# Kernel optimization log

Hardware: AMD Instinct MI355X
Metric: run time of the kernel (lower is better)

Reference implementation:

```python
import jax, jax.numpy as jnp
import numpy as np

HEADS = 4
LOCAL_CTX = 8  # local_attn_ctx (stride)


def _strided_transpose(x, n_ctx, local_ctx):
    # [B, n_ctx, E] -> reshape [B, n_ctx//local, local, E] -> swap -> [B, n_ctx, E]
    B, _, E = x.shape
    bT = n_ctx // local_ctx
    return x.reshape(B, bT, local_ctx, E).transpose(0, 2, 1, 3).reshape(B, n_ctx, E)


def _strided_untranspose(a, n_ctx, local_ctx):
    B, _, E = a.shape
    bT = n_ctx // local_ctx
    return a.reshape(B, local_ctx, bT, E).transpose(0, 2, 1, 3).reshape(B, n_ctx, E)


def setup_inputs() -> dict:
    key = jax.random.key(0)
    ks = jax.random.split(key, 6)
    B, T, E = 2048, 64, 256
    value = jax.random.normal(ks[0], (B, T, E), dtype=jnp.float32)
    k_in = jax.random.normal(ks[1], (B, T, E), dtype=jnp.float32)
    query = jax.random.normal(ks[2], (B, T, E), dtype=jnp.float32)
    mask = jnp.ones((B, T), dtype=jnp.int32)  # unused by the block
    W_ff = jax.random.normal(ks[3], (256, T * E), dtype=jnp.float32) * (1.0 / np.sqrt(T * E))
    b_ff = jax.random.normal(ks[4], (256,), dtype=jnp.float32) * 0.01
    return {"value": value, "key": k_in, "query": query, "mask": mask, "W_ff": W_ff, "b_ff": b_ff}


def reference(value, key, query, mask, W_ff, b_ff):
    B, n_ctx, E = query.shape
    # strided transpose of q, k, v
    q = _strided_transpose(query, n_ctx, LOCAL_CTX)
    k = _strided_transpose(key, n_ctx, LOCAL_CTX)
    v = _strided_transpose(value, n_ctx, LOCAL_CTX)
    scale = 1.0 / np.sqrt(E // HEADS)  # n_state = embd // heads
    w = jax.nn.softmax(jnp.einsum('bqe,bke->bqk', q, k) * scale, axis=-1)
    a = jnp.einsum('bqk,bke->bqe', w, v)
    attention = _strided_untranspose(a, n_ctx, LOCAL_CTX)
    # residual + dropout (eval-mode identity)
    x = attention + query
    # flatten-linear + ReLU
    out = jax.nn.relu(x.reshape(B, n_ctx * E) @ W_ff.T + b_ff)
    return (out, attention)
```

## Files before the change

kernel.cpp:

```cpp
#include <hip/hip_runtime.h>
#include <stdint.h>

typedef __attribute__((ext_vector_type(8))) short s16x8;
typedef __attribute__((ext_vector_type(8))) _Float16 h16x8;
typedef __attribute__((ext_vector_type(4))) float f32x4;

__device__ __forceinline__ unsigned short f2h_bits(float f) {
  union { _Float16 h; unsigned short u; } cv;
  cv.h = (_Float16)f;
  return cv.u;
}
__device__ __forceinline__ unsigned short f2bf(float f) {
  unsigned int u = __float_as_uint(f);
  u += 0x7fffu + ((u >> 16) & 1u);
  return (unsigned short)(u >> 16);
}
__device__ __forceinline__ f32x4 mfma16h(h16x8 a, h16x8 b, f32x4 c) {
  return __builtin_amdgcn_mfma_f32_16x16x32_f16(a, b, c, 0, 0, 0);
}

__device__ __forceinline__ void write_vq(char* VqB, int ep2, int tg, const float2* g) {
  s16x8 lo, hi;
#pragma unroll
  for (int j = 0; j < 8; ++j) {
    lo[j] = (short)f2h_bits(g[j].x);
    hi[j] = (short)f2h_bits(g[j].y);
  }
  *(s16x8*)(VqB + ep2 * 128 + ((16 * tg) ^ (((ep2 >> 1) & 7) << 4))) = lo;
  *(s16x8*)(VqB + (ep2 + 1) * 128 + ((16 * tg) ^ (((ep2 >> 1) & 7) << 4))) = hi;
}

__global__ __launch_bounds__(256) void attn_kernel(
    const float* __restrict__ Vg, const float* __restrict__ Kg,
    const float* __restrict__ Qg, float* __restrict__ attn_out,
    unsigned short* __restrict__ xb ) {
  __shared__ __align__(16) char smem[24576];
  char* PLB = smem + 16384;

  const int b = blockIdx.x;
  const int tid = threadIdx.x;
  const int lane = tid & 63;
  const int w = tid >> 6;
  const int n = lane & 15;
  const int q = lane >> 4;

  const float* Qb = Qg + (size_t)b * 64 * 256;
  const float* Kb = Kg + (size_t)b * 64 * 256;
  const float* Vb = Vg + (size_t)b * 64 * 256;

  const int ep2 = (tid & 31) * 2;
  const int tg = tid >> 5;

  f32x4 accS[4];
#pragma unroll
  for (int c = 0; c < 4; ++c) accS[c] = f32x4{0.f, 0.f, 0.f, 0.f};

#pragma unroll
  for (int ph = 0; ph < 2; ++ph) {
    const int e0 = ph * 128;
#pragma unroll
    for (int kk = 0; kk < 4; ++kk) {
      const int cb = kk * 32 + q * 8;
      const float* qsrc = Qb + (16 * w + n) * 256 + e0 + cb;
      float4 q0 = *(const float4*)qsrc;
      float4 q1 = *(const float4*)(qsrc + 4);
      float4 k0[4], k1[4];
#pragma unroll
      for (int c = 0; c < 4; ++c) {
        const float* ksrc = Kb + (16 * c + n) * 256 + e0 + cb;
        k0[c] = *(const float4*)ksrc;
        k1[c] = *(const float4*)(ksrc + 4);
      }
      h16x8 qh;
      qh[0] = (_Float16)q0.x; qh[1] = (_Float16)q0.y;
      qh[2] = (_Float16)q0.z; qh[3] = (_Float16)q0.w;
      qh[4] = (_Float16)q1.x; qh[5] = (_Float16)q1.y;
      qh[6] = (_Float16)q1.z; qh[7] = (_Float16)q1.w;
#pragma unroll
      for (int c = 0; c < 4; ++c) {
        h16x8 kh;
        kh[0] = (_Float16)k0[c].x; kh[1] = (_Float16)k0[c].y;
        kh[2] = (_Float16)k0[c].z; kh[3] = (_Float16)k0[c].w;
        kh[4] = (_Float16)k1[c].x; kh[5] = (_Float16)k1[c].y;
        kh[6] = (_Float16)k1[c].z; kh[7] = (_Float16)k1[c].w;
        accS[c] = mfma16h(qh, kh, accS[c]);
      }
    }
  }

  float2 g0[8], g1[8];
#pragma unroll
  for (int j = 0; j < 8; ++j) g0[j] = *(const float2*)(Vb + (tg * 8 + j) * 256 + 0 + ep2);
#pragma unroll
  for (int j = 0; j < 8; ++j) g1[j] = *(const float2*)(Vb + (tg * 8 + j) * 256 + 64 + ep2);

  const float scale = 0.125f;
  float p[4][4];
#pragma unroll
  for (int r = 0; r < 4; ++r) {
    float m = -1e30f;
#pragma unroll
    for (int c = 0; c < 4; ++c) m = fmaxf(m, accS[c][r]);
#pragma unroll
    for (int mk = 1; mk < 16; mk <<= 1) m = fmaxf(m, __shfl_xor(m, mk, 64));
    float s = 0.f;
#pragma unroll
    for (int c = 0; c < 4; ++c) {
      float e = __expf((accS[c][r] - m) * scale);
      p[c][r] = e;
      s += e;
    }
#pragma unroll
    for (int mk = 1; mk < 16; mk <<= 1) s += __shfl_xor(s, mk, 64);
    float inv = 1.0f / s;
#pragma unroll
    for (int c = 0; c < 4; ++c) p[c][r] *= inv;
  }

#pragma unroll
  for (int r = 0; r < 4; ++r) {
    int row = 16 * w + 4 * q + r;
    int sw = (row & 7) << 4;
#pragma unroll
    for (int c = 0; c < 4; ++c)
      *(unsigned short*)(PLB + row * 128 + ((2 * (16 * c + n)) ^ sw)) =
          f2h_bits(p[c][r]);
  }

  write_vq(smem, ep2, tg, g0);
  __syncthreads();

  float2 g2[8], g3[8];
  f32x4 accA[4];
#pragma unroll
  for (int qi = 0; qi < 4; ++qi) {
    char* VqB = smem + (qi & 1) * 8192;
    if (qi == 0) {
#pragma unroll
      for (int j = 0; j < 8; ++j)
        g2[j] = *(const float2*)(Vb + (tg * 8 + j) * 256 + 128 + ep2);
    }
    if (qi == 1) {
#pragma unroll
      for (int j = 0; j < 8; ++j)
        g3[j] = *(const float2*)(Vb + (tg * 8 + j) * 256 + 192 + ep2);
    }

#pragma unroll
    for (int c = 0; c < 4; ++c) accA[c] = f32x4{0.f, 0.f, 0.f, 0.f};
    __builtin_amdgcn_s_setprio(1);
#pragma unroll
    for (int ks = 0; ks < 2; ++ks) {
      const int cb = (ks * 32 + q * 8) * 2;
      h16x8 af = *(const h16x8*)(PLB + (16 * w + n) * 128 + (cb ^ ((n & 7) << 4)));
#pragma unroll
      for (int c = 0; c < 4; ++c) {
        int row = 16 * c + n;
        h16x8 bf = *(const h16x8*)(VqB + row * 128 + (cb ^ (((row >> 1) & 7) << 4)));
        accA[c] = mfma16h(af, bf, accA[c]);
      }
    }
    __builtin_amdgcn_s_setprio(0);

    if (qi < 3) {
      char* VqN = smem + ((qi + 1) & 1) * 8192;
      if (qi == 0) write_vq(VqN, ep2, tg, g1);
      if (qi == 1) write_vq(VqN, ep2, tg, g2);
      if (qi == 2) write_vq(VqN, ep2, tg, g3);
      __syncthreads();
    }

#pragma unroll
    for (int r = 0; r < 4; ++r) {
      int t = 16 * w + 4 * q + r;
      const float* qrow = Qb + t * 256 + qi * 64;
      size_t base = ((size_t)b * 64 + t) * 256 + qi * 64;
#pragma unroll
      for (int c = 0; c < 4; ++c) {
        int e = 16 * c + n;
        float aval = accA[c][r];
        attn_out[base + e] = aval;
        if (xb) xb[base + e] = f2h_bits(aval + qrow[e]);
      }
    }
  }
}

__global__ __launch_bounds__(256) void w2b_kernel(const float* __restrict__ W,
                                                  unsigned short* __restrict__ Wb) {
  int i = blockIdx.x * 256 + threadIdx.x;
  float4 v = ((const float4*)W)[i];
  ushort4 o;
  o.x = f2h_bits(v.x); o.y = f2h_bits(v.y); o.z = f2h_bits(v.z); o.w = f2h_bits(v.w);
  ((ushort4*)Wb)[i] = o;
}

template <bool USE_XB>
__global__ __launch_bounds__(256) void ff_kernel(
    const unsigned short* __restrict__ xb, const float* __restrict__ attn,
    const float* __restrict__ query, const unsigned short* __restrict__ Wb,
    float* __restrict__ part, int kchunk) {
  __shared__ __align__(16) unsigned short As[64 * 72];
  __shared__ __align__(16) unsigned short Bs[64 * 72];
  const int tid = threadIdx.x;
  const int lane = tid & 63, w = tid >> 6, n = lane & 15, q = lane >> 4;
  const int m0 = blockIdx.x * 64;
  const int n0 = blockIdx.y * 64;
  const int k0 = blockIdx.z * kchunk;

  f32x4 acc[4];
#pragma unroll
  for (int c = 0; c < 4; ++c) acc[c] = f32x4{0.f, 0.f, 0.f, 0.f};

  const int srow = tid >> 3;
  const int scol = (tid & 7) * 8;

  for (int kk = 0; kk < kchunk; kk += 64) {
#pragma unroll
    for (int rr = 0; rr < 2; ++rr) {
      int row = rr * 32 + srow;
      size_t ga = (size_t)(m0 + row) * 16384 + k0 + kk + scol;
      if (USE_XB) {
        *(uint4*)(As + row * 72 + scol) = *(const uint4*)(xb + ga);
      } else {
        float4 a0 = *(const float4*)(attn + ga);
        float4 a1 = *(const float4*)(attn + ga + 4);
        float4 q0 = *(const float4*)(query + ga);
        float4 q1 = *(const float4*)(query + ga + 4);
        ushort4 h0, h1;
        h0.x = f2h_bits(a0.x + q0.x); h0.y = f2h_bits(a0.y + q0.y);
        h0.z = f2h_bits(a0.z + q0.z); h0.w = f2h_bits(a0.w + q0.w);
        h1.x = f2h_bits(a1.x + q1.x); h1.y = f2h_bits(a1.y + q1.y);
        h1.z = f2h_bits(a1.z + q1.z); h1.w = f2h_bits(a1.w + q1.w);
        *(ushort4*)(As + row * 72 + scol) = h0;
        *(ushort4*)(As + row * 72 + scol + 4) = h1;
      }
      size_t gw = (size_t)(n0 + row) * 16384 + k0 + kk + scol;
      *(uint4*)(Bs + row * 72 + scol) = *(const uint4*)(Wb + gw);
    }
    __syncthreads();
#pragma unroll
    for (int ks = 0; ks < 2; ++ks) {
      const int colb = ks * 32 + q * 8;
      h16x8 af = *(const h16x8*)(As + (16 * w + n) * 72 + colb);
#pragma unroll
      for (int c = 0; c < 4; ++c) {
        h16x8 bf = *(const h16x8*)(Bs + (16 * c + n) * 72 + colb);
        acc[c] = mfma16h(af, bf, acc[c]);
      }
    }
    __syncthreads();
  }
#pragma unroll
  for (int r = 0; r < 4; ++r) {
    int m = m0 + 16 * w + 4 * q + r;
#pragma unroll
    for (int c = 0; c < 4; ++c) {
      int nn = n0 + 16 * c + n;
      part[((size_t)blockIdx.z * 2048 + m) * 256 + nn] = acc[c][r];
    }
  }
}

__global__ __launch_bounds__(256) void relu_kernel(const float* __restrict__ part,
                                                   const float* __restrict__ bias,
                                                   float* __restrict__ out, int KS) {
  int idx = blockIdx.x * 256 + threadIdx.x;
  float s = bias[idx & 255];
  for (int ks = 0; ks < KS; ++ks) s += part[(size_t)ks * 2048 * 256 + idx];
  out[idx] = fmaxf(s, 0.f);
}

extern "C" void kernel_launch(void* const* d_in, const int* in_sizes, int n_in,
                              void* d_out, int out_size, void* d_ws, size_t ws_size,
                              hipStream_t stream) {
  const float* value = (const float*)d_in[0];
  const float* key   = (const float*)d_in[1];
  const float* query = (const float*)d_in[2];
  const float* W_ff  = (const float*)d_in[4];
  const float* b_ff  = (const float*)d_in[5];

  float* out  = (float*)d_out;
  float* attn = out + (size_t)2048 * 256;

  const int KS = 4;
  const size_t wb_bytes   = (size_t)256 * 16384 * 2;
  const size_t part_bytes = (size_t)KS * 2048 * 256 * 4;
  const size_t xb_bytes   = (size_t)2048 * 64 * 256 * 2;
  unsigned short* Wb = (unsigned short*)d_ws;
  float* part = (float*)((char*)d_ws + wb_bytes);
  bool use_xb = ws_size >= wb_bytes + part_bytes + xb_bytes;
  unsigned short* xb =
      use_xb ? (unsigned short*)((char*)d_ws + wb_bytes + part_bytes) : nullptr;

  w2b_kernel<<<4096, 256, 0, stream>>>(W_ff, Wb);
  attn_kernel<<<2048, 256, 0, stream>>>(value, key, query, attn, xb);
  dim3 gb(32, 4, KS);
  if (use_xb)
    ff_kernel<true><<<gb, 256, 0, stream>>>(xb, nullptr, nullptr, Wb, part, 16384 / KS);
  else
    ff_kernel<false><<<gb, 256, 0, stream>>>(nullptr, attn, query, Wb, part, 16384 / KS);
  relu_kernel<<<2048, 256, 0, stream>>>(part, b_ff, out, KS);
}
```

Before: 285.6 us.

## Stage all of V in LDS early and double-buffer the FF GEMM tiles

The attention kernel now splits the QK^T loop into two halves and issues the V global loads between them. All four V quarters are written into a larger LDS buffer (40 KB) before the single barrier, which removes the per-quarter syncs and ping-pong writes in the PV loop. The feed-forward GEMM gets double-buffered LDS tiles with register prefetch of the next-next K tile, so there is one barrier per iteration instead of two and global loads overlap the MFMAs. The trade-off is more LDS per attention block, which can lower occupancy, and more registers held live in both kernels.

```diff
diff --git a/kernel.cpp b/kernel.cpp
--- a/kernel.cpp
+++ b/kernel.cpp
@@ -10,32 +10,28 @@
   cv.h = (_Float16)f;
   return cv.u;
 }
-__device__ __forceinline__ unsigned short f2bf(float f) {
-  unsigned int u = __float_as_uint(f);
-  u += 0x7fffu + ((u >> 16) & 1u);
-  return (unsigned short)(u >> 16);
-}
 __device__ __forceinline__ f32x4 mfma16h(h16x8 a, h16x8 b, f32x4 c) {
   return __builtin_amdgcn_mfma_f32_16x16x32_f16(a, b, c, 0, 0, 0);
 }
 
-__device__ __forceinline__ void write_vq(char* VqB, int ep2, int tg, const float2* g) {
+__device__ __forceinline__ void write_vq(char* base, int e, int tg, const float2* g) {
   s16x8 lo, hi;
 #pragma unroll
   for (int j = 0; j < 8; ++j) {
     lo[j] = (short)f2h_bits(g[j].x);
     hi[j] = (short)f2h_bits(g[j].y);
   }
-  *(s16x8*)(VqB + ep2 * 128 + ((16 * tg) ^ (((ep2 >> 1) & 7) << 4))) = lo;
-  *(s16x8*)(VqB + (ep2 + 1) * 128 + ((16 * tg) ^ (((ep2 >> 1) & 7) << 4))) = hi;
+  int sw = ((e >> 1) & 7) << 4;
+  *(s16x8*)(base + e * 128 + ((16 * tg) ^ sw)) = lo;
+  *(s16x8*)(base + (e + 1) * 128 + ((16 * tg) ^ sw)) = hi;
 }
 
 __global__ __launch_bounds__(256) void attn_kernel(
     const float* __restrict__ Vg, const float* __restrict__ Kg,
     const float* __restrict__ Qg, float* __restrict__ attn_out,
     unsigned short* __restrict__ xb ) {
-  __shared__ __align__(16) char smem[24576];
-  char* PLB = smem + 16384;
+  __shared__ __align__(16) char smem[40960];
+  char* PLB = smem + 32768;
 
   const int b = blockIdx.x;
   const int tid = threadIdx.x;
@@ -55,44 +51,79 @@
 #pragma unroll
   for (int c = 0; c < 4; ++c) accS[c] = f32x4{0.f, 0.f, 0.f, 0.f};
 
-#pragma unroll
-  for (int ph = 0; ph < 2; ++ph) {
-    const int e0 = ph * 128;
-#pragma unroll
-    for (int kk = 0; kk < 4; ++kk) {
-      const int cb = kk * 32 + q * 8;
-      const float* qsrc = Qb + (16 * w + n) * 256 + e0 + cb;
-      float4 q0 = *(const float4*)qsrc;
-      float4 q1 = *(const float4*)(qsrc + 4);
-      float4 k0[4], k1[4];
-#pragma unroll
-      for (int c = 0; c < 4; ++c) {
-        const float* ksrc = Kb + (16 * c + n) * 256 + e0 + cb;
-        k0[c] = *(const float4*)ksrc;
-        k1[c] = *(const float4*)(ksrc + 4);
-      }
-      h16x8 qh;
-      qh[0] = (_Float16)q0.x; qh[1] = (_Float16)q0.y;
-      qh[2] = (_Float16)q0.z; qh[3] = (_Float16)q0.w;
-      qh[4] = (_Float16)q1.x; qh[5] = (_Float16)q1.y;
-      qh[6] = (_Float16)q1.z; qh[7] = (_Float16)q1.w;
-#pragma unroll
-      for (int c = 0; c < 4; ++c) {
-        h16x8 kh;
-        kh[0] = (_Float16)k0[c].x; kh[1] = (_Float16)k0[c].y;
-        kh[2] = (_Float16)k0[c].z; kh[3] = (_Float16)k0[c].w;
-        kh[4] = (_Float16)k1[c].x; kh[5] = (_Float16)k1[c].y;
-        kh[6] = (_Float16)k1[c].z; kh[7] = (_Float16)k1[c].w;
-        accS[c] = mfma16h(qh, kh, accS[c]);
-      }
-    }
-  }
-
-  float2 g0[8], g1[8];
+  float2 g0[8];
 #pragma unroll
   for (int j = 0; j < 8; ++j) g0[j] = *(const float2*)(Vb + (tg * 8 + j) * 256 + 0 + ep2);
+
+#pragma unroll
+  for (int kk = 0; kk < 4; ++kk) {
+    const int cb = kk * 32 + q * 8;
+    const float* qsrc = Qb + (16 * w + n) * 256 + cb;
+    float4 q0 = *(const float4*)qsrc;
+    float4 q1 = *(const float4*)(qsrc + 4);
+    float4 k0[4], k1[4];
+#pragma unroll
+    for (int c = 0; c < 4; ++c) {
+      const float* ksrc = Kb + (16 * c + n) * 256 + cb;
+      k0[c] = *(const float4*)ksrc;
+      k1[c] = *(const float4*)(ksrc + 4);
+    }
+    h16x8 qh;
+    qh[0] = (_Float16)q0.x; qh[1] = (_Float16)q0.y;
+    qh[2] = (_Float16)q0.z; qh[3] = (_Float16)q0.w;
+    qh[4] = (_Float16)q1.x; qh[5] = (_Float16)q1.y;
+    qh[6] = (_Float16)q1.z; qh[7] = (_Float16)q1.w;
+#pragma unroll
+    for (int c = 0; c < 4; ++c) {
+      h16x8 kh;
+      kh[0] = (_Float16)k0[c].x; kh[1] = (_Float16)k0[c].y;
+      kh[2] = (_Float16)k0[c].z; kh[3] = (_Float16)k0[c].w;
+      kh[4] = (_Float16)k1[c].x; kh[5] = (_Float16)k1[c].y;
+      kh[6] = (_Float16)k1[c].z; kh[7] = (_Float16)k1[c].w;
+      accS[c] = mfma16h(qh, kh, accS[c]);
+    }
+  }
+
+  float2 g1[8];
 #pragma unroll
   for (int j = 0; j < 8; ++j) g1[j] = *(const float2*)(Vb + (tg * 8 + j) * 256 + 64 + ep2);
+
+#pragma unroll
+  for (int kk = 0; kk < 4; ++kk) {
+    const int cb = kk * 32 + q * 8;
+    const float* qsrc = Qb + (16 * w + n) * 256 + 128 + cb;
+    float4 q0 = *(const float4*)qsrc;
+    float4 q1 = *(const float4*)(qsrc + 4);
+    float4 k0[4], k1[4];
+#pragma unroll
+    for (int c = 0; c < 4; ++c) {
+      const float* ksrc = Kb + (16 * c + n) * 256 + 128 + cb;
+      k0[c] = *(const float4*)ksrc;
+      k1[c] = *(const float4*)(ksrc + 4);
+    }
+    h16x8 qh;
+    qh[0] = (_Float16)q0.x; qh[1] = (_Float16)q0.y;
+    qh[2] = (_Float16)q0.z; qh[3] = (_Float16)q0.w;
+    qh[4] = (_Float16)q1.x; qh[5] = (_Float16)q1.y;
+    qh[6] = (_Float16)q1.z; qh[7] = (_Float16)q1.w;
+#pragma unroll
+    for (int c = 0; c < 4; ++c) {
+      h16x8 kh;
+      kh[0] = (_Float16)k0[c].x; kh[1] = (_Float16)k0[c].y;
+      kh[2] = (_Float16)k0[c].z; kh[3] = (_Float16)k0[c].w;
+      kh[4] = (_Float16)k1[c].x; kh[5] = (_Float16)k1[c].y;
+      kh[6] = (_Float16)k1[c].z; kh[7] = (_Float16)k1[c].w;
+      accS[c] = mfma16h(qh, kh, accS[c]);
+    }
+  }
+
+  write_vq(smem, 0 + ep2, tg, g0);
+  write_vq(smem, 64 + ep2, tg, g1);
+  float2 g2[8], g3[8];
+#pragma unroll
+  for (int j = 0; j < 8; ++j) g2[j] = *(const float2*)(Vb + (tg * 8 + j) * 256 + 128 + ep2);
+#pragma unroll
+  for (int j = 0; j < 8; ++j) g3[j] = *(const float2*)(Vb + (tg * 8 + j) * 256 + 192 + ep2);
 
   const float scale = 0.125f;
   float p[4][4];
@@ -117,6 +148,9 @@
     for (int c = 0; c < 4; ++c) p[c][r] *= inv;
   }
 
+  write_vq(smem, 128 + ep2, tg, g2);
+  write_vq(smem, 192 + ep2, tg, g3);
+
 #pragma unroll
   for (int r = 0; r < 4; ++r) {
     int row = 16 * w + 4 * q + r;
@@ -127,25 +161,11 @@
           f2h_bits(p[c][r]);
   }
 
-  write_vq(smem, ep2, tg, g0);
   __syncthreads();
 
-  float2 g2[8], g3[8];
   f32x4 accA[4];
 #pragma unroll
   for (int qi = 0; qi < 4; ++qi) {
-    char* VqB = smem + (qi & 1) * 8192;
-    if (qi == 0) {
-#pragma unroll
-      for (int j = 0; j < 8; ++j)
-        g2[j] = *(const float2*)(Vb + (tg * 8 + j) * 256 + 128 + ep2);
-    }
-    if (qi == 1) {
-#pragma unroll
-      for (int j = 0; j < 8; ++j)
-        g3[j] = *(const float2*)(Vb + (tg * 8 + j) * 256 + 192 + ep2);
-    }
-
 #pragma unroll
     for (int c = 0; c < 4; ++c) accA[c] = f32x4{0.f, 0.f, 0.f, 0.f};
     __builtin_amdgcn_s_setprio(1);
@@ -155,20 +175,12 @@
       h16x8 af = *(const h16x8*)(PLB + (16 * w + n) * 128 + (cb ^ ((n & 7) << 4)));
 #pragma unroll
       for (int c = 0; c < 4; ++c) {
-        int row = 16 * c + n;
-        h16x8 bf = *(const h16x8*)(VqB + row * 128 + (cb ^ (((row >> 1) & 7) << 4)));
+        int row = qi * 64 + 16 * c + n;
+        h16x8 bf = *(const h16x8*)(smem + row * 128 + (cb ^ (((row >> 1) & 7) << 4)));
         accA[c] = mfma16h(af, bf, accA[c]);
       }
     }
     __builtin_amdgcn_s_setprio(0);
-
-    if (qi < 3) {
-      char* VqN = smem + ((qi + 1) & 1) * 8192;
-      if (qi == 0) write_vq(VqN, ep2, tg, g1);
-      if (qi == 1) write_vq(VqN, ep2, tg, g2);
-      if (qi == 2) write_vq(VqN, ep2, tg, g3);
-      __syncthreads();
-    }
 
 #pragma unroll
     for (int r = 0; r < 4; ++r) {
@@ -200,8 +212,8 @@
     const unsigned short* __restrict__ xb, const float* __restrict__ attn,
     const float* __restrict__ query, const unsigned short* __restrict__ Wb,
     float* __restrict__ part, int kchunk) {
-  __shared__ __align__(16) unsigned short As[64 * 72];
-  __shared__ __align__(16) unsigned short Bs[64 * 72];
+  __shared__ __align__(16) unsigned short As[2][64 * 72];
+  __shared__ __align__(16) unsigned short Bs[2][64 * 72];
   const int tid = threadIdx.x;
   const int lane = tid & 63, w = tid >> 6, n = lane & 15, q = lane >> 4;
   const int m0 = blockIdx.x * 64;
@@ -214,43 +226,81 @@
 
   const int srow = tid >> 3;
   const int scol = (tid & 7) * 8;
-
-  for (int kk = 0; kk < kchunk; kk += 64) {
-#pragma unroll
-    for (int rr = 0; rr < 2; ++rr) {
-      int row = rr * 32 + srow;
-      size_t ga = (size_t)(m0 + row) * 16384 + k0 + kk + scol;
-      if (USE_XB) {
-        *(uint4*)(As + row * 72 + scol) = *(const uint4*)(xb + ga);
-      } else {
-        float4 a0 = *(const float4*)(attn + ga);
-        float4 a1 = *(const float4*)(attn + ga + 4);
-        float4 q0 = *(const float4*)(query + ga);
-        float4 q1 = *(const float4*)(query + ga + 4);
-        ushort4 h0, h1;
-        h0.x = f2h_bits(a0.x + q0.x); h0.y = f2h_bits(a0.y + q0.y);
-        h0.z = f2h_bits(a0.z + q0.z); h0.w = f2h_bits(a0.w + q0.w);
-        h1.x = f2h_bits(a1.x + q1.x); h1.y = f2h_bits(a1.y + q1.y);
-        h1.z = f2h_bits(a1.z + q1.z); h1.w = f2h_bits(a1.w + q1.w);
-        *(ushort4*)(As + row * 72 + scol) = h0;
-        *(ushort4*)(As + row * 72 + scol + 4) = h1;
-      }
-      size_t gw = (size_t)(n0 + row) * 16384 + k0 + kk + scol;
-      *(uint4*)(Bs + row * 72 + scol) = *(const uint4*)(Wb + gw);
-    }
-    __syncthreads();
+  const int nIter = kchunk >> 6;
+
+  uint4 ra[2], rb[2];
+  float4 fa[2][2], fq[2][2];
+
+#define FF_LOAD(t)                                                   \
+  {                                                                  \
+    int kk = (t)*64;                                                 \
+    _Pragma("unroll") for (int rr = 0; rr < 2; ++rr) {               \
+      int row = rr * 32 + srow;                                      \
+      size_t ga = (size_t)(m0 + row) * 16384 + k0 + kk + scol;       \
+      if (USE_XB) {                                                  \
+        ra[rr] = *(const uint4*)(xb + ga);                           \
+      } else {                                                       \
+        fa[rr][0] = *(const float4*)(attn + ga);                     \
+        fa[rr][1] = *(const float4*)(attn + ga + 4);                 \
+        fq[rr][0] = *(const float4*)(query + ga);                    \
+        fq[rr][1] = *(const float4*)(query + ga + 4);                \
+      }                                                              \
+      size_t gw = (size_t)(n0 + row) * 16384 + k0 + kk + scol;       \
+      rb[rr] = *(const uint4*)(Wb + gw);                             \
+    }                                                                \
+  }
+
+#define FF_WRITE(bufi)                                               \
+  {                                                                  \
+    _Pragma("unroll") for (int rr = 0; rr < 2; ++rr) {               \
+      int row = rr * 32 + srow;                                      \
+      if (USE_XB) {                                                  \
+        *(uint4*)(&As[bufi][row * 72 + scol]) = ra[rr];              \
+      } else {                                                       \
+        ushort4 h0, h1;                                              \
+        h0.x = f2h_bits(fa[rr][0].x + fq[rr][0].x);                  \
+        h0.y = f2h_bits(fa[rr][0].y + fq[rr][0].y);                  \
+        h0.z = f2h_bits(fa[rr][0].z + fq[rr][0].z);                  \
+        h0.w = f2h_bits(fa[rr][0].w + fq[rr][0].w);                  \
+        h1.x = f2h_bits(fa[rr][1].x + fq[rr][1].x);                  \
+        h1.y = f2h_bits(fa[rr][1].y + fq[rr][1].y);                  \
+        h1.z = f2h_bits(fa[rr][1].z + fq[rr][1].z);                  \
+        h1.w = f2h_bits(fa[rr][1].w + fq[rr][1].w);                  \
+        *(ushort4*)(&As[bufi][row * 72 + scol]) = h0;                \
+        *(ushort4*)(&As[bufi][row * 72 + scol + 4]) = h1;            \
+      }                                                              \
+      *(uint4*)(&Bs[bufi][row * 72 + scol]) = rb[rr];                \
+    }                                                                \
+  }
+
+  FF_LOAD(0);
+  FF_WRITE(0);
+  FF_LOAD(1);
+  asm volatile("s_waitcnt lgkmcnt(0)" ::: "memory");
+  __builtin_amdgcn_s_barrier();
+
+  for (int t = 0; t < nIter; ++t) {
+    const int cur = t & 1;
 #pragma unroll
     for (int ks = 0; ks < 2; ++ks) {
       const int colb = ks * 32 + q * 8;
-      h16x8 af = *(const h16x8*)(As + (16 * w + n) * 72 + colb);
+      h16x8 af = *(const h16x8*)(&As[cur][(16 * w + n) * 72 + colb]);
 #pragma unroll
       for (int c = 0; c < 4; ++c) {
-        h16x8 bf = *(const h16x8*)(Bs + (16 * c + n) * 72 + colb);
+        h16x8 bf = *(const h16x8*)(&Bs[cur][(16 * c + n) * 72 + colb]);
         acc[c] = mfma16h(af, bf, acc[c]);
       }
     }
-    __syncthreads();
-  }
+    if (t + 1 < nIter) {
+      FF_WRITE(cur ^ 1);
+      if (t + 2 < nIter) FF_LOAD(t + 2);
+      asm volatile("s_waitcnt lgkmcnt(0)" ::: "memory");
+      __builtin_amdgcn_s_barrier();
+    }
+  }
+#undef FF_LOAD
+#undef FF_WRITE
+
 #pragma unroll
   for (int r = 0; r < 4; ++r) {
     int m = m0 + 16 * w + 4 * q + r;
```

New measurement: 331.3 us. 1.16x slower.

## Stage K through LDS with async global_load_lds and keep full V^T resident

Applied to the files above, without the earlier changes.

K tiles are now copied into a double-buffered LDS region with asynchronous global-to-LDS loads, four 64-column quarters, so QK^T reads K from LDS rather than each wave reloading all of K from global memory. All of V is converted into a 32 KB LDS transpose before PV, which removes the per-quarter barriers and rewrites. Shared memory rises to 64 KB with launch_bounds(256,2), so occupancy is capped at two blocks per CU and more barriers are added during the QK phase.

```diff
diff --git a/kernel.cpp b/kernel.cpp
--- a/kernel.cpp
+++ b/kernel.cpp
@@ -10,32 +10,77 @@
   cv.h = (_Float16)f;
   return cv.u;
 }
-__device__ __forceinline__ unsigned short f2bf(float f) {
-  unsigned int u = __float_as_uint(f);
-  u += 0x7fffu + ((u >> 16) & 1u);
-  return (unsigned short)(u >> 16);
-}
 __device__ __forceinline__ f32x4 mfma16h(h16x8 a, h16x8 b, f32x4 c) {
   return __builtin_amdgcn_mfma_f32_16x16x32_f16(a, b, c, 0, 0, 0);
 }
 
-__device__ __forceinline__ void write_vq(char* VqB, int ep2, int tg, const float2* g) {
+typedef const unsigned int __attribute__((address_space(1)))* as1_u32p;
+typedef unsigned int __attribute__((address_space(3)))* as3_u32p;
+__device__ __forceinline__ void async_ld16(const void* g, void* l) {
+  __builtin_amdgcn_global_load_lds((as1_u32p)g, (as3_u32p)l, 16, 0, 0);
+}
+
+__device__ __forceinline__ void stage_kq(char* buf, const float* Kb, int qi,
+                                         int w, int lane) {
+#pragma unroll
+  for (int i = 0; i < 4; ++i) {
+    int seg = w * 4 + i;
+    int row = seg * 4 + (lane >> 4);
+    int sg = (lane & 15) ^ (row & 7);
+    async_ld16(Kb + row * 256 + qi * 64 + sg * 4, buf + seg * 1024);
+  }
+}
+
+__device__ __forceinline__ void qk_quarter(const char* buf, const float* Qb, int qi,
+                                           int w, int n, int q, f32x4* accS) {
+#pragma unroll
+  for (int kkl = 0; kkl < 2; ++kkl) {
+    const float* qsrc = Qb + (16 * w + n) * 256 + qi * 64 + kkl * 32 + q * 8;
+    float4 q0 = *(const float4*)qsrc;
+    float4 q1 = *(const float4*)(qsrc + 4);
+    h16x8 qh;
+    qh[0] = (_Float16)q0.x; qh[1] = (_Float16)q0.y;
+    qh[2] = (_Float16)q0.z; qh[3] = (_Float16)q0.w;
+    qh[4] = (_Float16)q1.x; qh[5] = (_Float16)q1.y;
+    qh[6] = (_Float16)q1.z; qh[7] = (_Float16)q1.w;
+    const int g = kkl * 8 + q * 2;
+#pragma unroll
+    for (int c = 0; c < 4; ++c) {
+      int row = 16 * c + n;
+      int s = row & 7;
+      float4 k0 = *(const float4*)(buf + row * 256 + ((g ^ s) * 16));
+      float4 k1 = *(const float4*)(buf + row * 256 + (((g + 1) ^ s) * 16));
+      h16x8 kh;
+      kh[0] = (_Float16)k0.x; kh[1] = (_Float16)k0.y;
+      kh[2] = (_Float16)k0.z; kh[3] = (_Float16)k0.w;
+      kh[4] = (_Float16)k1.x; kh[5] = (_Float16)k1.y;
+      kh[6] = (_Float16)k1.z; kh[7] = (_Float16)k1.w;
+      accS[c] = mfma16h(qh, kh, accS[c]);
+    }
+  }
+}
+
+__device__ __forceinline__ void write_vq(char* base, int e, int tg, const float2* g) {
   s16x8 lo, hi;
 #pragma unroll
   for (int j = 0; j < 8; ++j) {
     lo[j] = (short)f2h_bits(g[j].x);
     hi[j] = (short)f2h_bits(g[j].y);
   }
-  *(s16x8*)(VqB + ep2 * 128 + ((16 * tg) ^ (((ep2 >> 1) & 7) << 4))) = lo;
-  *(s16x8*)(VqB + (ep2 + 1) * 128 + ((16 * tg) ^ (((ep2 >> 1) & 7) << 4))) = hi;
-}
-
-__global__ __launch_bounds__(256) void attn_kernel(
+  int sw = ((e >> 1) & 7) << 4;
+  *(s16x8*)(base + e * 128 + ((16 * tg) ^ sw)) = lo;
+  *(s16x8*)(base + (e + 1) * 128 + ((16 * tg) ^ sw)) = hi;
+}
+
+__global__ __launch_bounds__(256, 2) void attn_kernel(
     const float* __restrict__ Vg, const float* __restrict__ Kg,
     const float* __restrict__ Qg, float* __restrict__ attn_out,
     unsigned short* __restrict__ xb ) {
-  __shared__ __align__(16) char smem[24576];
-  char* PLB = smem + 16384;
+  __shared__ __align__(16) char smem[65536];
+  char* b0 = smem;
+  char* b1 = smem + 16384;
+  char* Vt = smem + 32768;
+  char* PLB = smem;
 
   const int b = blockIdx.x;
   const int tid = threadIdx.x;
@@ -55,44 +100,34 @@
 #pragma unroll
   for (int c = 0; c < 4; ++c) accS[c] = f32x4{0.f, 0.f, 0.f, 0.f};
 
-#pragma unroll
-  for (int ph = 0; ph < 2; ++ph) {
-    const int e0 = ph * 128;
-#pragma unroll
-    for (int kk = 0; kk < 4; ++kk) {
-      const int cb = kk * 32 + q * 8;
-      const float* qsrc = Qb + (16 * w + n) * 256 + e0 + cb;
-      float4 q0 = *(const float4*)qsrc;
-      float4 q1 = *(const float4*)(qsrc + 4);
-      float4 k0[4], k1[4];
-#pragma unroll
-      for (int c = 0; c < 4; ++c) {
-        const float* ksrc = Kb + (16 * c + n) * 256 + e0 + cb;
-        k0[c] = *(const float4*)ksrc;
-        k1[c] = *(const float4*)(ksrc + 4);
-      }
-      h16x8 qh;
-      qh[0] = (_Float16)q0.x; qh[1] = (_Float16)q0.y;
-      qh[2] = (_Float16)q0.z; qh[3] = (_Float16)q0.w;
-      qh[4] = (_Float16)q1.x; qh[5] = (_Float16)q1.y;
-      qh[6] = (_Float16)q1.z; qh[7] = (_Float16)q1.w;
-#pragma unroll
-      for (int c = 0; c < 4; ++c) {
-        h16x8 kh;
-        kh[0] = (_Float16)k0[c].x; kh[1] = (_Float16)k0[c].y;
-        kh[2] = (_Float16)k0[c].z; kh[3] = (_Float16)k0[c].w;
-        kh[4] = (_Float16)k1[c].x; kh[5] = (_Float16)k1[c].y;
-        kh[6] = (_Float16)k1[c].z; kh[7] = (_Float16)k1[c].w;
-        accS[c] = mfma16h(qh, kh, accS[c]);
-      }
-    }
-  }
-
+  stage_kq(b0, Kb, 0, w, lane);
+  stage_kq(b1, Kb, 1, w, lane);
   float2 g0[8], g1[8];
 #pragma unroll
   for (int j = 0; j < 8; ++j) g0[j] = *(const float2*)(Vb + (tg * 8 + j) * 256 + 0 + ep2);
 #pragma unroll
   for (int j = 0; j < 8; ++j) g1[j] = *(const float2*)(Vb + (tg * 8 + j) * 256 + 64 + ep2);
+  __syncthreads();
+
+  write_vq(Vt, 0 + ep2, tg, g0);
+  write_vq(Vt, 64 + ep2, tg, g1);
+  float2 g2[8], g3[8];
+#pragma unroll
+  for (int j = 0; j < 8; ++j) g2[j] = *(const float2*)(Vb + (tg * 8 + j) * 256 + 128 + ep2);
+#pragma unroll
+  for (int j = 0; j < 8; ++j) g3[j] = *(const float2*)(Vb + (tg * 8 + j) * 256 + 192 + ep2);
+
+  qk_quarter(b0, Qb, 0, w, n, q, accS);
+  __syncthreads();
+  stage_kq(b0, Kb, 2, w, lane);
+  qk_quarter(b1, Qb, 1, w, n, q, accS);
+  __syncthreads();
+  stage_kq(b1, Kb, 3, w, lane);
+  write_vq(Vt, 128 + ep2, tg, g2);
+  write_vq(Vt, 192 + ep2, tg, g3);
+  qk_quarter(b0, Qb, 2, w, n, q, accS);
+  __syncthreads();
+  qk_quarter(b1, Qb, 3, w, n, q, accS);
 
   const float scale = 0.125f;
   float p[4][4];
@@ -127,25 +162,11 @@
           f2h_bits(p[c][r]);
   }
 
-  write_vq(smem, ep2, tg, g0);
-  __syncthreads();
-
-  float2 g2[8], g3[8];
+  __syncthreads();
+
   f32x4 accA[4];
 #pragma unroll
   for (int qi = 0; qi < 4; ++qi) {
-    char* VqB = smem + (qi & 1) * 8192;
-    if (qi == 0) {
-#pragma unroll
-      for (int j = 0; j < 8; ++j)
-        g2[j] = *(const float2*)(Vb + (tg * 8 + j) * 256 + 128 + ep2);
-    }
-    if (qi == 1) {
-#pragma unroll
-      for (int j = 0; j < 8; ++j)
-        g3[j] = *(const float2*)(Vb + (tg * 8 + j) * 256 + 192 + ep2);
-    }
-
 #pragma unroll
     for (int c = 0; c < 4; ++c) accA[c] = f32x4{0.f, 0.f, 0.f, 0.f};
     __builtin_amdgcn_s_setprio(1);
@@ -155,20 +176,12 @@
       h16x8 af = *(const h16x8*)(PLB + (16 * w + n) * 128 + (cb ^ ((n & 7) << 4)));
 #pragma unroll
       for (int c = 0; c < 4; ++c) {
-        int row = 16 * c + n;
-        h16x8 bf = *(const h16x8*)(VqB + row * 128 + (cb ^ (((row >> 1) & 7) << 4)));
+        int row = qi * 64 + 16 * c + n;
+        h16x8 bf = *(const h16x8*)(Vt + row * 128 + (cb ^ (((row >> 1) & 7) << 4)));
         accA[c] = mfma16h(af, bf, accA[c]);
       }
     }
     __builtin_amdgcn_s_setprio(0);
-
-    if (qi < 3) {
-      char* VqN = smem + ((qi + 1) & 1) * 8192;
-      if (qi == 0) write_vq(VqN, ep2, tg, g1);
-      if (qi == 1) write_vq(VqN, ep2, tg, g2);
-      if (qi == 2) write_vq(VqN, ep2, tg, g3);
-      __syncthreads();
-    }
 
 #pragma unroll
     for (int r = 0; r < 4; ++r) {
```

Measured after the change: 280.3 us. Within noise of the previous version (-1.9%).

## Process two batches per attention block and drop LDS staging in FF GEMM

Applied to the files above, without the earlier changes.

The attention kernel now handles two batch items per block. Their QK^T MFMAs are interleaved, and the V-chunk double-buffered pipeline runs over 8 chunks, so fewer blocks run longer with more memory-level parallelism. The FF GEMM no longer stages tiles through shared memory and reads MFMA fragments straight from global memory. Its blocks are remapped with an XCD-aware swizzle so that blocks sharing tiles land together in L2. The trade-offs are higher register and LDS use, fewer blocks for latency hiding, and possibly uncoalesced direct global fragment loads in the GEMM.

```diff
diff --git a/kernel.cpp b/kernel.cpp
--- a/kernel.cpp
+++ b/kernel.cpp
@@ -10,13 +10,22 @@
   cv.h = (_Float16)f;
   return cv.u;
 }
-__device__ __forceinline__ unsigned short f2bf(float f) {
-  unsigned int u = __float_as_uint(f);
-  u += 0x7fffu + ((u >> 16) & 1u);
-  return (unsigned short)(u >> 16);
-}
 __device__ __forceinline__ f32x4 mfma16h(h16x8 a, h16x8 b, f32x4 c) {
   return __builtin_amdgcn_mfma_f32_16x16x32_f16(a, b, c, 0, 0, 0);
+}
+__device__ __forceinline__ h16x8 cvt8(float4 x, float4 y) {
+  h16x8 r;
+  r[0] = (_Float16)x.x; r[1] = (_Float16)x.y; r[2] = (_Float16)x.z; r[3] = (_Float16)x.w;
+  r[4] = (_Float16)y.x; r[5] = (_Float16)y.y; r[6] = (_Float16)y.z; r[7] = (_Float16)y.w;
+  return r;
+}
+__device__ __forceinline__ h16x8 cvt8s(float4 x, float4 y, float4 u, float4 v) {
+  h16x8 r;
+  r[0] = (_Float16)(x.x + u.x); r[1] = (_Float16)(x.y + u.y);
+  r[2] = (_Float16)(x.z + u.z); r[3] = (_Float16)(x.w + u.w);
+  r[4] = (_Float16)(y.x + v.x); r[5] = (_Float16)(y.y + v.y);
+  r[6] = (_Float16)(y.z + v.z); r[7] = (_Float16)(y.w + v.w);
+  return r;
 }
 
 __device__ __forceinline__ void write_vq(char* VqB, int ep2, int tg, const float2* g) {
@@ -26,95 +35,124 @@
     lo[j] = (short)f2h_bits(g[j].x);
     hi[j] = (short)f2h_bits(g[j].y);
   }
-  *(s16x8*)(VqB + ep2 * 128 + ((16 * tg) ^ (((ep2 >> 1) & 7) << 4))) = lo;
-  *(s16x8*)(VqB + (ep2 + 1) * 128 + ((16 * tg) ^ (((ep2 >> 1) & 7) << 4))) = hi;
-}
+  int sw = ((ep2 >> 1) & 7) << 4;
+  *(s16x8*)(VqB + ep2 * 128 + ((16 * tg) ^ sw)) = lo;
+  *(s16x8*)(VqB + (ep2 + 1) * 128 + ((16 * tg) ^ sw)) = hi;
+}
+
+#define GATH(arr, Vsrc, qq)                                            \
+  _Pragma("unroll") for (int j = 0; j < 8; ++j) arr[j] =               \
+      *(const float2*)((Vsrc) + (tg * 8 + j) * 256 + (qq)*64 + ep2);
 
 __global__ __launch_bounds__(256) void attn_kernel(
     const float* __restrict__ Vg, const float* __restrict__ Kg,
     const float* __restrict__ Qg, float* __restrict__ attn_out,
     unsigned short* __restrict__ xb ) {
-  __shared__ __align__(16) char smem[24576];
-  char* PLB = smem + 16384;
-
-  const int b = blockIdx.x;
+  __shared__ __align__(16) char smem[32768];
+  char* PLA = smem + 16384;
+  char* PLB2 = smem + 24576;
+
+  const int b0 = blockIdx.x * 2;
   const int tid = threadIdx.x;
   const int lane = tid & 63;
   const int w = tid >> 6;
   const int n = lane & 15;
   const int q = lane >> 4;
 
-  const float* Qb = Qg + (size_t)b * 64 * 256;
-  const float* Kb = Kg + (size_t)b * 64 * 256;
-  const float* Vb = Vg + (size_t)b * 64 * 256;
+  const float* QA = Qg + (size_t)b0 * 64 * 256;
+  const float* KA = Kg + (size_t)b0 * 64 * 256;
+  const float* VA = Vg + (size_t)b0 * 64 * 256;
+  const float* QB = QA + 64 * 256;
+  const float* KB = KA + 64 * 256;
+  const float* VB = VA + 64 * 256;
 
   const int ep2 = (tid & 31) * 2;
   const int tg = tid >> 5;
 
-  f32x4 accS[4];
-#pragma unroll
-  for (int c = 0; c < 4; ++c) accS[c] = f32x4{0.f, 0.f, 0.f, 0.f};
+  f32x4 sA[4], sB[4];
+#pragma unroll
+  for (int c = 0; c < 4; ++c) {
+    sA[c] = f32x4{0.f, 0.f, 0.f, 0.f};
+    sB[c] = f32x4{0.f, 0.f, 0.f, 0.f};
+  }
 
 #pragma unroll
   for (int ph = 0; ph < 2; ++ph) {
-    const int e0 = ph * 128;
 #pragma unroll
     for (int kk = 0; kk < 4; ++kk) {
-      const int cb = kk * 32 + q * 8;
-      const float* qsrc = Qb + (16 * w + n) * 256 + e0 + cb;
-      float4 q0 = *(const float4*)qsrc;
-      float4 q1 = *(const float4*)(qsrc + 4);
-      float4 k0[4], k1[4];
-#pragma unroll
-      for (int c = 0; c < 4; ++c) {
-        const float* ksrc = Kb + (16 * c + n) * 256 + e0 + cb;
-        k0[c] = *(const float4*)ksrc;
-        k1[c] = *(const float4*)(ksrc + 4);
-      }
-      h16x8 qh;
-      qh[0] = (_Float16)q0.x; qh[1] = (_Float16)q0.y;
-      qh[2] = (_Float16)q0.z; qh[3] = (_Float16)q0.w;
-      qh[4] = (_Float16)q1.x; qh[5] = (_Float16)q1.y;
-      qh[6] = (_Float16)q1.z; qh[7] = (_Float16)q1.w;
-#pragma unroll
-      for (int c = 0; c < 4; ++c) {
-        h16x8 kh;
-        kh[0] = (_Float16)k0[c].x; kh[1] = (_Float16)k0[c].y;
-        kh[2] = (_Float16)k0[c].z; kh[3] = (_Float16)k0[c].w;
-        kh[4] = (_Float16)k1[c].x; kh[5] = (_Float16)k1[c].y;
-        kh[6] = (_Float16)k1[c].z; kh[7] = (_Float16)k1[c].w;
-        accS[c] = mfma16h(qh, kh, accS[c]);
-      }
-    }
-  }
-
-  float2 g0[8], g1[8];
-#pragma unroll
-  for (int j = 0; j < 8; ++j) g0[j] = *(const float2*)(Vb + (tg * 8 + j) * 256 + 0 + ep2);
-#pragma unroll
-  for (int j = 0; j < 8; ++j) g1[j] = *(const float2*)(Vb + (tg * 8 + j) * 256 + 64 + ep2);
+      const int cb = ph * 128 + kk * 32 + q * 8;
+      const float* qa = QA + (16 * w + n) * 256 + cb;
+      const float* qb = QB + (16 * w + n) * 256 + cb;
+      float4 a0 = *(const float4*)qa, a1 = *(const float4*)(qa + 4);
+      float4 e0 = *(const float4*)qb, e1 = *(const float4*)(qb + 4);
+      float4 ka0[4], ka1[4], kb0[4], kb1[4];
+#pragma unroll
+      for (int c = 0; c < 4; ++c) {
+        const float* ks = KA + (16 * c + n) * 256 + cb;
+        ka0[c] = *(const float4*)ks;
+        ka1[c] = *(const float4*)(ks + 4);
+      }
+#pragma unroll
+      for (int c = 0; c < 4; ++c) {
+        const float* ks = KB + (16 * c + n) * 256 + cb;
+        kb0[c] = *(const float4*)ks;
+        kb1[c] = *(const float4*)(ks + 4);
+      }
+      h16x8 qha = cvt8(a0, a1);
+      h16x8 qhb = cvt8(e0, e1);
+#pragma unroll
+      for (int c = 0; c < 4; ++c) {
+        sA[c] = mfma16h(qha, cvt8(ka0[c], ka1[c]), sA[c]);
+        sB[c] = mfma16h(qhb, cvt8(kb0[c], kb1[c]), sB[c]);
+      }
+    }
+  }
+
+  float2 arrA[8], arrB[8];
+  GATH(arrA, VA, 0);
+  GATH(arrB, VA, 1);
 
   const float scale = 0.125f;
-  float p[4][4];
+  float pA[4][4], pB[4][4];
 #pragma unroll
   for (int r = 0; r < 4; ++r) {
     float m = -1e30f;
 #pragma unroll
-    for (int c = 0; c < 4; ++c) m = fmaxf(m, accS[c][r]);
+    for (int c = 0; c < 4; ++c) m = fmaxf(m, sA[c][r]);
 #pragma unroll
     for (int mk = 1; mk < 16; mk <<= 1) m = fmaxf(m, __shfl_xor(m, mk, 64));
     float s = 0.f;
 #pragma unroll
     for (int c = 0; c < 4; ++c) {
-      float e = __expf((accS[c][r] - m) * scale);
-      p[c][r] = e;
+      float e = __expf((sA[c][r] - m) * scale);
+      pA[c][r] = e;
       s += e;
     }
 #pragma unroll
     for (int mk = 1; mk < 16; mk <<= 1) s += __shfl_xor(s, mk, 64);
     float inv = 1.0f / s;
 #pragma unroll
-    for (int c = 0; c < 4; ++c) p[c][r] *= inv;
+    for (int c = 0; c < 4; ++c) pA[c][r] *= inv;
+  }
+#pragma unroll
+  for (int r = 0; r < 4; ++r) {
+    float m = -1e30f;
+#pragma unroll
+    for (int c = 0; c < 4; ++c) m = fmaxf(m, sB[c][r]);
+#pragma unroll
+    for (int mk = 1; mk < 16; mk <<= 1) m = fmaxf(m, __shfl_xor(m, mk, 64));
+    float s = 0.f;
+#pragma unroll
+    for (int c = 0; c < 4; ++c) {
+      float e = __expf((sB[c][r] - m) * scale);
+      pB[c][r] = e;
+      s += e;
+    }
+#pragma unroll
+    for (int mk = 1; mk < 16; mk <<= 1) s += __shfl_xor(s, mk, 64);
+    float inv = 1.0f / s;
+#pragma unroll
+    for (int c = 0; c < 4; ++c) pB[c][r] *= inv;
   }
 
 #pragma unroll
@@ -122,59 +160,61 @@
     int row = 16 * w + 4 * q + r;
     int sw = (row & 7) << 4;
 #pragma unroll
-    for (int c = 0; c < 4; ++c)
-      *(unsigned short*)(PLB + row * 128 + ((2 * (16 * c + n)) ^ sw)) =
-          f2h_bits(p[c][r]);
-  }
-
-  write_vq(smem, ep2, tg, g0);
+    for (int c = 0; c < 4; ++c) {
+      *(unsigned short*)(PLA + row * 128 + ((2 * (16 * c + n)) ^ sw)) =
+          f2h_bits(pA[c][r]);
+      *(unsigned short*)(PLB2 + row * 128 + ((2 * (16 * c + n)) ^ sw)) =
+          f2h_bits(pB[c][r]);
+    }
+  }
+
+  write_vq(smem, ep2, tg, arrA);
+  GATH(arrA, VA, 2);
   __syncthreads();
 
-  float2 g2[8], g3[8];
   f32x4 accA[4];
 #pragma unroll
-  for (int qi = 0; qi < 4; ++qi) {
-    char* VqB = smem + (qi & 1) * 8192;
-    if (qi == 0) {
-#pragma unroll
-      for (int j = 0; j < 8; ++j)
-        g2[j] = *(const float2*)(Vb + (tg * 8 + j) * 256 + 128 + ep2);
-    }
-    if (qi == 1) {
-#pragma unroll
-      for (int j = 0; j < 8; ++j)
-        g3[j] = *(const float2*)(Vb + (tg * 8 + j) * 256 + 192 + ep2);
-    }
-
+  for (int i = 0; i < 8; ++i) {
+    char* bufc = smem + (i & 1) * 8192;
+    const char* PL = (i < 4) ? PLA : PLB2;
 #pragma unroll
     for (int c = 0; c < 4; ++c) accA[c] = f32x4{0.f, 0.f, 0.f, 0.f};
     __builtin_amdgcn_s_setprio(1);
 #pragma unroll
     for (int ks = 0; ks < 2; ++ks) {
       const int cb = (ks * 32 + q * 8) * 2;
-      h16x8 af = *(const h16x8*)(PLB + (16 * w + n) * 128 + (cb ^ ((n & 7) << 4)));
+      h16x8 af = *(const h16x8*)(PL + (16 * w + n) * 128 + (cb ^ ((n & 7) << 4)));
 #pragma unroll
       for (int c = 0; c < 4; ++c) {
         int row = 16 * c + n;
-        h16x8 bf = *(const h16x8*)(VqB + row * 128 + (cb ^ (((row >> 1) & 7) << 4)));
+        h16x8 bf = *(const h16x8*)(bufc + row * 128 + (cb ^ (((row >> 1) & 7) << 4)));
         accA[c] = mfma16h(af, bf, accA[c]);
       }
     }
     __builtin_amdgcn_s_setprio(0);
 
-    if (qi < 3) {
-      char* VqN = smem + ((qi + 1) & 1) * 8192;
-      if (qi == 0) write_vq(VqN, ep2, tg, g1);
-      if (qi == 1) write_vq(VqN, ep2, tg, g2);
-      if (qi == 2) write_vq(VqN, ep2, tg, g3);
+    if (i < 7) {
       __syncthreads();
-    }
-
+      char* bufn = smem + ((i + 1) & 1) * 8192;
+      if ((i + 1) & 1) write_vq(bufn, ep2, tg, arrB);
+      else             write_vq(bufn, ep2, tg, arrA);
+      if (i + 3 < 8) {
+        const float* src = (i + 3 < 4) ? VA : VB;
+        const int qq = (i + 3) & 3;
+        if ((i + 1) & 1) { GATH(arrB, src, qq); }
+        else             { GATH(arrA, src, qq); }
+      }
+      __syncthreads();
+    }
+
+    const float* Qe = (i < 4) ? QA : QB;
+    const size_t bb = (size_t)((i < 4) ? b0 : b0 + 1);
+    const int ql = i & 3;
 #pragma unroll
     for (int r = 0; r < 4; ++r) {
       int t = 16 * w + 4 * q + r;
-      const float* qrow = Qb + t * 256 + qi * 64;
-      size_t base = ((size_t)b * 64 + t) * 256 + qi * 64;
+      const float* qrow = Qe + t * 256 + ql * 64;
+      size_t base = (bb * 64 + t) * 256 + ql * 64;
 #pragma unroll
       for (int c = 0; c < 4; ++c) {
         int e = 16 * c + n;
@@ -199,65 +239,51 @@
 __global__ __launch_bounds__(256) void ff_kernel(
     const unsigned short* __restrict__ xb, const float* __restrict__ attn,
     const float* __restrict__ query, const unsigned short* __restrict__ Wb,
-    float* __restrict__ part, int kchunk) {
-  __shared__ __align__(16) unsigned short As[64 * 72];
-  __shared__ __align__(16) unsigned short Bs[64 * 72];
+    float* __restrict__ part) {
   const int tid = threadIdx.x;
   const int lane = tid & 63, w = tid >> 6, n = lane & 15, q = lane >> 4;
-  const int m0 = blockIdx.x * 64;
-  const int n0 = blockIdx.y * 64;
-  const int k0 = blockIdx.z * kchunk;
+  const int p = blockIdx.x;
+  const int l = (p & 7) * 64 + (p >> 3);
+  const int m0 = (l & 31) * 64;
+  const int n0 = ((l >> 5) & 3) * 64;
+  const int z = l >> 7;
+  const int k0 = z * 4096;
 
   f32x4 acc[4];
 #pragma unroll
   for (int c = 0; c < 4; ++c) acc[c] = f32x4{0.f, 0.f, 0.f, 0.f};
 
-  const int srow = tid >> 3;
-  const int scol = (tid & 7) * 8;
-
-  for (int kk = 0; kk < kchunk; kk += 64) {
-#pragma unroll
-    for (int rr = 0; rr < 2; ++rr) {
-      int row = rr * 32 + srow;
-      size_t ga = (size_t)(m0 + row) * 16384 + k0 + kk + scol;
-      if (USE_XB) {
-        *(uint4*)(As + row * 72 + scol) = *(const uint4*)(xb + ga);
-      } else {
-        float4 a0 = *(const float4*)(attn + ga);
-        float4 a1 = *(const float4*)(attn + ga + 4);
-        float4 q0 = *(const float4*)(query + ga);
-        float4 q1 = *(const float4*)(query + ga + 4);
-        ushort4 h0, h1;
-        h0.x = f2h_bits(a0.x + q0.x); h0.y = f2h_bits(a0.y + q0.y);
-        h0.z = f2h_bits(a0.z + q0.z); h0.w = f2h_bits(a0.w + q0.w);
-        h1.x = f2h_bits(a1.x + q1.x); h1.y = f2h_bits(a1.y + q1.y);
-        h1.z = f2h_bits(a1.z + q1.z); h1.w = f2h_bits(a1.w + q1.w);
-        *(ushort4*)(As + row * 72 + scol) = h0;
-        *(ushort4*)(As + row * 72 + scol + 4) = h1;
-      }
-      size_t gw = (size_t)(n0 + row) * 16384 + k0 + kk + scol;
-      *(uint4*)(Bs + row * 72 + scol) = *(const uint4*)(Wb + gw);
-    }
-    __syncthreads();
-#pragma unroll
-    for (int ks = 0; ks < 2; ++ks) {
-      const int colb = ks * 32 + q * 8;
-      h16x8 af = *(const h16x8*)(As + (16 * w + n) * 72 + colb);
-#pragma unroll
-      for (int c = 0; c < 4; ++c) {
-        h16x8 bf = *(const h16x8*)(Bs + (16 * c + n) * 72 + colb);
-        acc[c] = mfma16h(af, bf, acc[c]);
-      }
-    }
-    __syncthreads();
-  }
+  const size_t ar = (size_t)(m0 + 16 * w + n) * 16384 + k0 + q * 8;
+  size_t br[4];
+#pragma unroll
+  for (int c = 0; c < 4; ++c) br[c] = (size_t)(n0 + 16 * c + n) * 16384 + k0 + q * 8;
+
+#pragma unroll 4
+  for (int kp = 0; kp < 4096; kp += 32) {
+    h16x8 af;
+    if (USE_XB) {
+      af = *(const h16x8*)(xb + ar + kp);
+    } else {
+      const float* ap = attn + ar + kp;
+      const float* qp = query + ar + kp;
+      float4 x0 = *(const float4*)ap, x1 = *(const float4*)(ap + 4);
+      float4 y0 = *(const float4*)qp, y1 = *(const float4*)(qp + 4);
+      af = cvt8s(x0, x1, y0, y1);
+    }
+#pragma unroll
+    for (int c = 0; c < 4; ++c) {
+      h16x8 bf = *(const h16x8*)(Wb + br[c] + kp);
+      acc[c] = mfma16h(af, bf, acc[c]);
+    }
+  }
+
 #pragma unroll
   for (int r = 0; r < 4; ++r) {
     int m = m0 + 16 * w + 4 * q + r;
 #pragma unroll
     for (int c = 0; c < 4; ++c) {
       int nn = n0 + 16 * c + n;
-      part[((size_t)blockIdx.z * 2048 + m) * 256 + nn] = acc[c][r];
+      part[((size_t)z * 2048 + m) * 256 + nn] = acc[c][r];
     }
   }
 }
@@ -294,11 +320,10 @@
       use_xb ? (unsigned short*)((char*)d_ws + wb_bytes + part_bytes) : nullptr;
 
   w2b_kernel<<<4096, 256, 0, stream>>>(W_ff, Wb);
-  attn_kernel<<<2048, 256, 0, stream>>>(value, key, query, attn, xb);
-  dim3 gb(32, 4, KS);
+  attn_kernel<<<1024, 256, 0, stream>>>(value, key, query, attn, xb);
   if (use_xb)
-    ff_kernel<true><<<gb, 256, 0, stream>>>(xb, nullptr, nullptr, Wb, part, 16384 / KS);
+    ff_kernel<true><<<512, 256, 0, stream>>>(xb, nullptr, nullptr, Wb, part);
   else
-    ff_kernel<false><<<gb, 256, 0, stream>>>(nullptr, attn, query, Wb, part, 16384 / KS);
+    ff_kernel<false><<<512, 256, 0, stream>>>(nullptr, attn, query, Wb, part);
   relu_kernel<<<2048, 256, 0, stream>>>(part, b_ff, out, KS);
 }
```

New measurement: 339.0 us. +18.7%, slower.
